# Kernel tuning notes

Measured on AMD Instinct MI355X. Metric: run time of the kernel, lower is better.

Reference implementation:

```python
import jax, jax.numpy as jnp
import numpy as np

LD, LU, N, D_IN, D_OUT, K = 16384, 65536, 8, 256, 128, 3


def setup_inputs() -> dict:
    key = jax.random.key(0)
    ks = jax.random.split(key, 7)
    down_features = jax.random.normal(ks[0], (LD, N, D_IN), dtype=jnp.float32)
    up_features = jax.random.normal(ks[1], (LU, N, D_OUT), dtype=jnp.float32)
    idx = jax.random.randint(ks[2], (LU, N, K), 0, LD, dtype=jnp.int32)
    W1 = jax.random.normal(ks[3], (D_IN, D_OUT), dtype=jnp.float32) / np.sqrt(D_IN)
    b1 = jnp.zeros((D_OUT,), dtype=jnp.float32)
    W2 = jax.random.normal(ks[4], (D_OUT, D_OUT), dtype=jnp.float32) / np.sqrt(D_OUT)
    b2 = jnp.zeros((D_OUT,), dtype=jnp.float32)
    return {"down_features": down_features, "up_features": up_features, "idx": idx,
            "W1": W1, "b1": b1, "W2": W2, "b2": b2}


def reference(down_features, up_features, idx, W1, b1, W2, b2):
    # MLP: Linear(d, d_out) -> ReLU -> Linear(d_out, d_out), applied per point
    h = jax.nn.relu(jnp.einsum("lnd,de->lne", down_features, W1) + b1)
    h = jnp.einsum("lnd,de->lne", h, W2) + b2            # (Ld, N, Du)
    # KNN upsample: gather K neighbors per upsampled point, average, residual add
    n = jnp.arange(h.shape[1])[None, :, None]            # (1, N, 1) batch index
    gathered = h[idx, n, :]                              # (Lu, N, K, Du)
    up = up_features + gathered.mean(axis=2)             # (Lu, N, Du)
    return up
```

## Files before the change

kernel.cpp:

```cpp
#include <hip/hip_runtime.h>

#define LD_   16384
#define LU_   65536
#define N_    8
#define DIN   256
#define DOUT  128
#define K_    3
#define M_    (LD_ * N_)

typedef short bf16x8 __attribute__((ext_vector_type(8)));
typedef float f32x4  __attribute__((ext_vector_type(4)));
typedef unsigned int u32x2 __attribute__((ext_vector_type(2)));

__device__ __forceinline__ unsigned short f2bf(float f) {
    unsigned int x = __float_as_uint(f);
    x += 0x7fffu + ((x >> 16) & 1u);
    return (unsigned short)(x >> 16);
}

__device__ __forceinline__ bf16x8 ld_bf16x8(const unsigned short* p) {
    const short4 lo = *(const short4*)p;
    const short4 hi = *(const short4*)(p + 4);
    bf16x8 r = {lo.x, lo.y, lo.z, lo.w, hi.x, hi.y, hi.z, hi.w};
    return r;
}

#define W1_STRIDE 260
#define W2_STRIDE 132
#define H1_STRIDE 132

__global__ __launch_bounds__(512, 2) void knn_mlp_mfma(
    const float* __restrict__ down, const float* __restrict__ W1,
    const float* __restrict__ b1,   const float* __restrict__ W2,
    const float* __restrict__ b2,   unsigned short* __restrict__ h)
{
    __shared__ unsigned short sW1t[DOUT * W1_STRIDE];
    __shared__ unsigned short sW2t[DOUT * W2_STRIDE];
    __shared__ unsigned short sH[8][16 * H1_STRIDE];
    __shared__ float sB1[DOUT], sB2[DOUT];

    const int tid  = threadIdx.x;
    const int wave = tid >> 6, lane = tid & 63;
    const int lm = lane & 15, lg = lane >> 4;

    const int row0 = blockIdx.x * 512 + wave * 16;
    const float* dbase = down + (size_t)(row0 + lm) * DIN + lg * 8;

    float4 raw[16];
    #pragma unroll
    for (int k = 0; k < 8; ++k) {
        raw[2 * k]     = *(const float4*)(dbase + k * 32);
        raw[2 * k + 1] = *(const float4*)(dbase + k * 32 + 4);
    }

    #pragma unroll
    for (int it = 0; it < 16; ++it) {
        const int fid = it * 512 + tid;
        const int k = fid >> 5, n4 = (fid & 31) * 4;
        const float4 w = ((const float4*)W1)[fid];
        sW1t[(n4 + 0) * W1_STRIDE + k] = f2bf(w.x);
        sW1t[(n4 + 1) * W1_STRIDE + k] = f2bf(w.y);
        sW1t[(n4 + 2) * W1_STRIDE + k] = f2bf(w.z);
        sW1t[(n4 + 3) * W1_STRIDE + k] = f2bf(w.w);
    }
    #pragma unroll
    for (int it = 0; it < 8; ++it) {
        const int fid = it * 512 + tid;
        const int k = fid >> 5, n4 = (fid & 31) * 4;
        const float4 w = ((const float4*)W2)[fid];
        sW2t[(n4 + 0) * W2_STRIDE + k] = f2bf(w.x);
        sW2t[(n4 + 1) * W2_STRIDE + k] = f2bf(w.y);
        sW2t[(n4 + 2) * W2_STRIDE + k] = f2bf(w.z);
        sW2t[(n4 + 3) * W2_STRIDE + k] = f2bf(w.w);
    }
    if (tid < 32)      ((float4*)sB1)[tid]      = ((const float4*)b1)[tid];
    else if (tid < 64) ((float4*)sB2)[tid - 32] = ((const float4*)b2)[tid - 32];
    __syncthreads();

    unsigned short* hw = sH[wave];

    #pragma unroll
    for (int pass = 0; pass < 4; ++pass) {
        const int chunk = row0 + pass * 128;

        bf16x8 A[8];
        #pragma unroll
        for (int k = 0; k < 8; ++k) {
            const float4 r0 = raw[2 * k], r1 = raw[2 * k + 1];
            const bf16x8 a = {(short)f2bf(r0.x), (short)f2bf(r0.y), (short)f2bf(r0.z), (short)f2bf(r0.w),
                              (short)f2bf(r1.x), (short)f2bf(r1.y), (short)f2bf(r1.z), (short)f2bf(r1.w)};
            A[k] = a;
        }

        if (pass < 3) {
            const float* dp = dbase + (size_t)(pass + 1) * 128 * DIN;
            #pragma unroll
            for (int k = 0; k < 8; ++k) {
                raw[2 * k]     = *(const float4*)(dp + k * 32);
                raw[2 * k + 1] = *(const float4*)(dp + k * 32 + 4);
            }
        }

        f32x4 acc[8];
        #pragma unroll
        for (int nt = 0; nt < 8; ++nt) acc[nt] = (f32x4){0.f, 0.f, 0.f, 0.f};
        #pragma unroll
        for (int k = 0; k < 8; ++k) {
            const int koff = k * 32 + lg * 8;
            #pragma unroll
            for (int nt = 0; nt < 8; ++nt) {
                const bf16x8 Wf = ld_bf16x8(&sW1t[(nt * 16 + lm) * W1_STRIDE + koff]);
                acc[nt] = __builtin_amdgcn_mfma_f32_16x16x32_bf16(Wf, A[k], acc[nt], 0, 0, 0);
            }
        }

        #pragma unroll
        for (int nt = 0; nt < 8; ++nt) {
            const float4 bq = *(const float4*)&sB1[nt * 16 + lg * 4];
            ushort4 st;
            st.x = f2bf(fmaxf(acc[nt][0] + bq.x, 0.0f));
            st.y = f2bf(fmaxf(acc[nt][1] + bq.y, 0.0f));
            st.z = f2bf(fmaxf(acc[nt][2] + bq.z, 0.0f));
            st.w = f2bf(fmaxf(acc[nt][3] + bq.w, 0.0f));
            *(ushort4*)&hw[lm * H1_STRIDE + nt * 16 + lg * 4] = st;
        }
        asm volatile("s_waitcnt lgkmcnt(0)" ::: "memory");

        f32x4 acc2[8];
        #pragma unroll
        for (int nt = 0; nt < 8; ++nt) acc2[nt] = (f32x4){0.f, 0.f, 0.f, 0.f};
        #pragma unroll
        for (int ks = 0; ks < 4; ++ks) {
            const int koff = ks * 32 + lg * 8;
            const bf16x8 Bh = ld_bf16x8(&hw[lm * H1_STRIDE + koff]);
            #pragma unroll
            for (int nt = 0; nt < 8; ++nt) {
                const bf16x8 Wf = ld_bf16x8(&sW2t[(nt * 16 + lm) * W2_STRIDE + koff]);
                acc2[nt] = __builtin_amdgcn_mfma_f32_16x16x32_bf16(Wf, Bh, acc2[nt], 0, 0, 0);
            }
        }

        #pragma unroll
        for (int nt = 0; nt < 8; ++nt) {
            const float4 bq = *(const float4*)&sB2[nt * 16 + lg * 4];
            ushort4 st;
            st.x = f2bf(acc2[nt][0] + bq.x);
            st.y = f2bf(acc2[nt][1] + bq.y);
            st.z = f2bf(acc2[nt][2] + bq.z);
            st.w = f2bf(acc2[nt][3] + bq.w);
            *(ushort4*)&h[(size_t)(chunk + lm) * DOUT + nt * 16 + lg * 4] = st;
        }
    }
}

__global__ __launch_bounds__(256) void knn_gather(
    const float* __restrict__ up, const int* __restrict__ idx,
    const unsigned int* __restrict__ h32, float* __restrict__ out)
{
    const int wave = threadIdx.x >> 6, lane = threadIdx.x & 63;
    const int half = lane >> 5, lih = lane & 31;
    const long long wid  = (long long)blockIdx.x * 4 + wave;
    const long long base = wid * 64;

    const int* ip = idx + (base + lane) * 3;
    const int mi0 = ip[0], mi1 = ip[1], mi2 = ip[2];

    const u32x2* hg   = (const u32x2*)h32;
    const f32x4* upv  = (const f32x4*)up;
    f32x4*       outv = (f32x4*)out;

    #pragma unroll
    for (int gb = 0; gb < 8; ++gb) {
        u32x2 ga[4][3];
        f32x4 uu[4];
        int   pp[4];
        #pragma unroll
        for (int u = 0; u < 4; ++u) {
            const int p = (gb * 4 + u) * 2 + half;
            pp[u] = p;
            const int i0 = __shfl(mi0, p);
            const int i1 = __shfl(mi1, p);
            const int i2 = __shfl(mi2, p);
            const int n  = p & 7;
            ga[u][0] = hg[(unsigned)(i0 * 8 + n) * 32u + lih];
            ga[u][1] = hg[(unsigned)(i1 * 8 + n) * 32u + lih];
            ga[u][2] = hg[(unsigned)(i2 * 8 + n) * 32u + lih];
            uu[u] = __builtin_nontemporal_load(&upv[(base + p) * 32 + lih]);
        }
        #pragma unroll
        for (int u = 0; u < 4; ++u) {
            float s0 = 0.f, s1 = 0.f, s2 = 0.f, s3 = 0.f;
            #pragma unroll
            for (int j = 0; j < 3; ++j) {
                const u32x2 v = ga[u][j];
                s0 += __uint_as_float(v.x << 16);
                s1 += __uint_as_float(v.x & 0xffff0000u);
                s2 += __uint_as_float(v.y << 16);
                s3 += __uint_as_float(v.y & 0xffff0000u);
            }
            f32x4 o;
            o.x = uu[u].x + s0 * (1.0f / 3.0f);
            o.y = uu[u].y + s1 * (1.0f / 3.0f);
            o.z = uu[u].z + s2 * (1.0f / 3.0f);
            o.w = uu[u].w + s3 * (1.0f / 3.0f);
            __builtin_nontemporal_store(o, &outv[(base + pp[u]) * 32 + lih]);
        }
    }
}

extern "C" void kernel_launch(void* const* d_in, const int* in_sizes, int n_in,
                              void* d_out, int out_size, void* d_ws, size_t ws_size,
                              hipStream_t stream)
{
    const float* down = (const float*)d_in[0];
    const float* up   = (const float*)d_in[1];
    const int*   idx  = (const int*)d_in[2];
    const float* W1   = (const float*)d_in[3];
    const float* b1   = (const float*)d_in[4];
    const float* W2   = (const float*)d_in[5];
    const float* b2   = (const float*)d_in[6];
    float* out = (float*)d_out;
    unsigned short* h = (unsigned short*)d_ws;

    knn_mlp_mfma<<<256, 512, 0, stream>>>(down, W1, b1, W2, b2, h);
    knn_gather<<<2048, 256, 0, stream>>>(up, idx, (const unsigned int*)h, out);
}
```

Before: 556.9 us.

## Permute bf16 h layout for 16-byte gathers and double-buffer gather loads

The MLP kernel now writes h with permuted columns, so each 16-byte chunk holds column pairs c and c+64. The gather kernel can then fetch 8 bf16 values per lane with 16-lane groups covering a row. It also loads both halves of the up/out row per lane and uses a two-stage software pipeline over 16 row groups. The aim is fewer, wider gather transactions and better latency hiding. The cost is a more complex index mapping and higher register use, with occupancy hinted at 8 blocks.

```diff
diff --git a/kernel.cpp b/kernel.cpp
--- a/kernel.cpp
+++ b/kernel.cpp
@@ -10,7 +10,7 @@
 
 typedef short bf16x8 __attribute__((ext_vector_type(8)));
 typedef float f32x4  __attribute__((ext_vector_type(4)));
-typedef unsigned int u32x2 __attribute__((ext_vector_type(2)));
+typedef unsigned int u32x4 __attribute__((ext_vector_type(4)));
 
 __device__ __forceinline__ unsigned short f2bf(float f) {
     unsigned int x = __float_as_uint(f);
@@ -28,6 +28,7 @@
 #define W1_STRIDE 260
 #define W2_STRIDE 132
 #define H1_STRIDE 132
+
 
 __global__ __launch_bounds__(512, 2) void knn_mlp_mfma(
     const float* __restrict__ down, const float* __restrict__ W1,
@@ -148,63 +149,82 @@
             st.y = f2bf(acc2[nt][1] + bq.y);
             st.z = f2bf(acc2[nt][2] + bq.z);
             st.w = f2bf(acc2[nt][3] + bq.w);
-            *(ushort4*)&h[(size_t)(chunk + lm) * DOUT + nt * 16 + lg * 4] = st;
-        }
-    }
-}
-
-__global__ __launch_bounds__(256) void knn_gather(
+            const int c0   = nt * 16 + lg * 4;
+            const int soff = ((c0 & 63) << 1) + ((c0 >> 6) << 2);
+            *(ushort4*)&h[(size_t)(chunk + lm) * DOUT + soff] = st;
+        }
+    }
+}
+
+#define LOADG(g, g0, g1, g2, u0, u1, row) do {                               \
+    const int rr_ = (g) * 4 + q;                                             \
+    row = base + rr_;                                                        \
+    const int n_  = rr_ & 7;                              \
+    const int i0_ = __shfl(mi0, rr_);                                        \
+    const int i1_ = __shfl(mi1, rr_);                                        \
+    const int i2_ = __shfl(mi2, rr_);                                        \
+    g0 = hq[(unsigned)(i0_ * 8 + n_) * 16u + lq];                            \
+    g1 = hq[(unsigned)(i1_ * 8 + n_) * 16u + lq];                            \
+    g2 = hq[(unsigned)(i2_ * 8 + n_) * 16u + lq];                            \
+    u0 = __builtin_nontemporal_load(&upv[row * 32 + lq]);                    \
+    u1 = __builtin_nontemporal_load(&upv[row * 32 + 16 + lq]);               \
+} while (0)
+
+#define CONSUME(g0, g1, g2, u0, u1, row) do {                                \
+    float s0 = 0.f, s1 = 0.f, s2 = 0.f, s3 = 0.f;                            \
+    float s4 = 0.f, s5 = 0.f, s6 = 0.f, s7 = 0.f;                            \
+    const u32x4 ga_[3] = {g0, g1, g2};                                       \
+    _Pragma("unroll")                                                        \
+    for (int j = 0; j < 3; ++j) {                                            \
+        const u32x4 v = ga_[j];                                              \
+        s0 += __uint_as_float(v.x << 16);                                    \
+        s1 += __uint_as_float(v.x & 0xffff0000u);                            \
+        s2 += __uint_as_float(v.y << 16);                                    \
+        s3 += __uint_as_float(v.y & 0xffff0000u);                            \
+        s4 += __uint_as_float(v.z << 16);                                    \
+        s5 += __uint_as_float(v.z & 0xffff0000u);                            \
+        s6 += __uint_as_float(v.w << 16);                                    \
+        s7 += __uint_as_float(v.w & 0xffff0000u);                            \
+    }                                                                        \
+    f32x4 o0, o1;                                                            \
+    o0.x = u0.x + s0 * (1.0f / 3.0f);                                        \
+    o0.y = u0.y + s1 * (1.0f / 3.0f);                                        \
+    o0.z = u0.z + s2 * (1.0f / 3.0f);                                        \
+    o0.w = u0.w + s3 * (1.0f / 3.0f);                                        \
+    o1.x = u1.x + s4 * (1.0f / 3.0f);                                        \
+    o1.y = u1.y + s5 * (1.0f / 3.0f);                                        \
+    o1.z = u1.z + s6 * (1.0f / 3.0f);                                        \
+    o1.w = u1.w + s7 * (1.0f / 3.0f);                                        \
+    __builtin_nontemporal_store(o0, &outv[row * 32 + lq]);                   \
+    __builtin_nontemporal_store(o1, &outv[row * 32 + 16 + lq]);              \
+} while (0)
+
+__global__ __launch_bounds__(256, 8) void knn_gather(
     const float* __restrict__ up, const int* __restrict__ idx,
-    const unsigned int* __restrict__ h32, float* __restrict__ out)
+    const u32x4* __restrict__ hq, float* __restrict__ out)
 {
     const int wave = threadIdx.x >> 6, lane = threadIdx.x & 63;
-    const int half = lane >> 5, lih = lane & 31;
+    const int q = lane >> 4, lq = lane & 15;
     const long long wid  = (long long)blockIdx.x * 4 + wave;
     const long long base = wid * 64;
 
     const int* ip = idx + (base + lane) * 3;
     const int mi0 = ip[0], mi1 = ip[1], mi2 = ip[2];
 
-    const u32x2* hg   = (const u32x2*)h32;
     const f32x4* upv  = (const f32x4*)up;
     f32x4*       outv = (f32x4*)out;
 
-    #pragma unroll
-    for (int gb = 0; gb < 8; ++gb) {
-        u32x2 ga[4][3];
-        f32x4 uu[4];
-        int   pp[4];
-        #pragma unroll
-        for (int u = 0; u < 4; ++u) {
-            const int p = (gb * 4 + u) * 2 + half;
-            pp[u] = p;
-            const int i0 = __shfl(mi0, p);
-            const int i1 = __shfl(mi1, p);
-            const int i2 = __shfl(mi2, p);
-            const int n  = p & 7;
-            ga[u][0] = hg[(unsigned)(i0 * 8 + n) * 32u + lih];
-            ga[u][1] = hg[(unsigned)(i1 * 8 + n) * 32u + lih];
-            ga[u][2] = hg[(unsigned)(i2 * 8 + n) * 32u + lih];
-            uu[u] = __builtin_nontemporal_load(&upv[(base + p) * 32 + lih]);
-        }
-        #pragma unroll
-        for (int u = 0; u < 4; ++u) {
-            float s0 = 0.f, s1 = 0.f, s2 = 0.f, s3 = 0.f;
-            #pragma unroll
-            for (int j = 0; j < 3; ++j) {
-                const u32x2 v = ga[u][j];
-                s0 += __uint_as_float(v.x << 16);
-                s1 += __uint_as_float(v.x & 0xffff0000u);
-                s2 += __uint_as_float(v.y << 16);
-                s3 += __uint_as_float(v.y & 0xffff0000u);
-            }
-            f32x4 o;
-            o.x = uu[u].x + s0 * (1.0f / 3.0f);
-            o.y = uu[u].y + s1 * (1.0f / 3.0f);
-            o.z = uu[u].z + s2 * (1.0f / 3.0f);
-            o.w = uu[u].w + s3 * (1.0f / 3.0f);
-            __builtin_nontemporal_store(o, &outv[(base + pp[u]) * 32 + lih]);
-        }
+    u32x4 gA0, gA1, gA2, gB0, gB1, gB2;
+    f32x4 uA0, uA1, uB0, uB1;
+    long long rowA, rowB;
+
+    LOADG(0, gA0, gA1, gA2, uA0, uA1, rowA);
+    #pragma unroll
+    for (int g = 0; g < 16; g += 2) {
+        LOADG(g + 1, gB0, gB1, gB2, uB0, uB1, rowB);
+        CONSUME(gA0, gA1, gA2, uA0, uA1, rowA);
+        if (g + 2 < 16) LOADG(g + 2, gA0, gA1, gA2, uA0, uA1, rowA);
+        CONSUME(gB0, gB1, gB2, uB0, uB1, rowB);
     }
 }
 
@@ -223,5 +243,5 @@
     unsigned short* h = (unsigned short*)d_ws;
 
     knn_mlp_mfma<<<256, 512, 0, stream>>>(down, W1, b1, W2, b2, h);
-    knn_gather<<<2048, 256, 0, stream>>>(up, idx, (const unsigned int*)h, out);
-}
+    knn_gather<<<2048, 256, 0, stream>>>(up, idx, (const u32x4*)h, out);
+}
```

New measurement: 563.6 us. Within noise of the previous version (+1.2%).
